# Performance work log

Measured on AMD Instinct MI355X. Metric: run time of the kernel, lower is better.

The kernel has to match this reference:

```python
import jax, jax.numpy as jnp
import numpy as np

HEADS = 16
DIM_HEAD = 64
QUERY_DIM = 1024
CONTEXT_DIM = 1024
INNER = HEADS * DIM_HEAD  # 1024


def setup_inputs() -> dict:
    key = jax.random.key(0)
    k1, k2, k3, k4, k5, k6, k7 = jax.random.split(key, 7)
    b, nq, nk = 2, 2048, 2048
    q = jax.random.normal(k1, (b, nq, QUERY_DIM), dtype=jnp.float32)
    context = jax.random.normal(k2, (b, nk, CONTEXT_DIM), dtype=jnp.float32)
    # True = masked out (filled with -inf); keep sparse so no row is fully masked
    mask = jax.random.randint(k3, (b, nk), 0, 2).astype(bool) & jax.random.randint(k7, (b, nk), 0, 2).astype(bool)
    s = 0.02
    Wq = jax.random.normal(k4, (QUERY_DIM, INNER), dtype=jnp.float32) * s
    Wkv = jax.random.normal(k5, (CONTEXT_DIM, 2 * INNER), dtype=jnp.float32) * s
    Wout = jax.random.normal(k6, (INNER, QUERY_DIM), dtype=jnp.float32) * s
    b_out = jnp.zeros((QUERY_DIM,), dtype=jnp.float32)
    return {"q": q, "context": context, "mask": mask, "Wq": Wq, "Wkv": Wkv, "Wout": Wout, "b_out": b_out}


def reference(q, context, mask, Wq, Wkv, Wout, b_out):
    b, nq, _ = q.shape
    nk = context.shape[1]
    h, dh = HEADS, DIM_HEAD
    scale = dh ** -0.5
    qp = q @ Wq                              # [b, nq, h*dh]
    k, v = jnp.split(context @ Wkv, 2, -1)   # each [b, nk, h*dh]
    qh = qp.reshape(b, nq, h, dh).transpose(0, 2, 1, 3)  # [b, h, nq, dh]
    kh = k.reshape(b, nk, h, dh).transpose(0, 2, 1, 3)
    vh = v.reshape(b, nk, h, dh).transpose(0, 2, 1, 3)
    attn = jnp.einsum('bhid,bhjd->bhij', qh, kh) * scale  # [b, h, nq, nk]
    attn = jnp.where(mask[:, None, None, :], -jnp.inf, attn)
    attn = jax.nn.softmax(attn, axis=-1)
    out = jnp.einsum('bhij,bhjd->bhid', attn, vh)         # [b, h, nq, dh]
    out = out.transpose(0, 2, 1, 3).reshape(b, nq, h * dh)
    return out @ Wout + b_out
```

## Files before the change

### kernel.cpp

```cpp
#include <hip/hip_runtime.h>
#include <hip/hip_bf16.h>
#include <stdint.h>
#include <math.h>

typedef unsigned short u16;
typedef __attribute__((ext_vector_type(8))) short bf16x8;
typedef __attribute__((ext_vector_type(4))) float f32x4;
typedef __attribute__((ext_vector_type(16))) float f32x16;
typedef __attribute__((ext_vector_type(4))) u16 u16x4;

#define DEVI __device__ __forceinline__

DEVI u16 f2bf(float x){
  uint32_t u = __float_as_uint(x);
  u += 0x7fffu + ((u >> 16) & 1u);
  return (u16)(u >> 16);
}

DEVI uint32_t pkbf2(float lo, float hi){
  union { __hip_bfloat162 h; uint32_t u; } x;
  x.h.x = __float2bfloat16(lo);
  x.h.y = __float2bfloat16(hi);
  return x.u;
}

DEVI void gload_lds16(const void* g, void* l){
  __builtin_amdgcn_global_load_lds((__attribute__((address_space(1))) const void*)g,
                                   (__attribute__((address_space(3))) void*)l,
                                   16, 0, 0);
}

DEVI void pl32swap_u(uint32_t& a, uint32_t& b){
  asm volatile("v_permlane32_swap_b32 %0, %1" : "+&v"(a), "+v"(b));
}

__global__ __launch_bounds__(256) void k_prep(const float* __restrict__ q,
                                              const float* __restrict__ ctx,
                                              const int* __restrict__ m,
                                              u16* __restrict__ qb, u16* __restrict__ cb,
                                              uint32_t* __restrict__ mb){
  const int b = blockIdx.x;
  if (b < 2048){
    const float* s = (b < 1024) ? q : ctx;
    u16* d = (b < 1024) ? qb : cb;
    const int base = (b & 1023) << 12;
    #pragma unroll
    for (int it = 0; it < 4; ++it){
      const int i = base + (it << 10) + (threadIdx.x << 2);
      const float4 v = *(const float4*)(s + i);
      u16x4 o = { f2bf(v.x), f2bf(v.y), f2bf(v.z), f2bf(v.w) };
      *(u16x4*)(d + i) = o;
    }
  } else {
    for (int w = threadIdx.x; w < 128; w += 256){
      const int bb = w >> 6, wi = w & 63;
      uint32_t bits = 0;
      for (int i = 0; i < 32; ++i) bits |= (m[(bb << 11) + (wi << 5) + i] ? 1u : 0u) << i;
      mb[w] = bits;
    }
  }
}

__global__ __launch_bounds__(256) void k_tr3(const float* __restrict__ Wq,
                                             const float* __restrict__ Wkv,
                                             const float* __restrict__ Wo,
                                             u16* __restrict__ WqT, u16* __restrict__ WkvT,
                                             u16* __restrict__ WoT){
  const int z = blockIdx.z;
  if (z != 1 && blockIdx.x >= 16) return;
  const float* s = (z == 0) ? Wq : (z == 1) ? Wkv : Wo;
  u16* d = (z == 0) ? WqT : (z == 1) ? WkvT : WoT;
  const int R = 1024, C = (z == 1) ? 2048 : 1024;
  __shared__ float t[64][65];
  const int x = threadIdx.x, y = threadIdx.y;
  const int r0 = blockIdx.y * 64, c0 = blockIdx.x * 64;
  #pragma unroll
  for (int yy = y; yy < 64; yy += 4) t[yy][x] = s[(size_t)(r0 + yy) * C + c0 + x];
  __syncthreads();
  #pragma unroll
  for (int yy = y; yy < 64; yy += 4) d[(size_t)(c0 + yy) * R + r0 + x] = f2bf(t[x][yy]);
}

__global__ __launch_bounds__(256, 2)
void k_gemm01(const u16* __restrict__ Aq, const u16* __restrict__ Ac,
              const u16* __restrict__ Bq, const u16* __restrict__ Bkv,
              u16* __restrict__ QPb, u16* __restrict__ Kbb, u16* __restrict__ Vtb)
{
  __shared__ __align__(16) u16 As[128 * 64];
  __shared__ __align__(16) u16 Bs[128 * 64];
  const int tid = threadIdx.x;
  const int lane = tid & 63, wave = tid >> 6;
  const int g = lane >> 4, l16 = lane & 15;
  const int bx = blockIdx.x;
  const bool isq = bx < 8;
  const u16* A = isq ? Aq : Ac;
  const u16* B = isq ? Bq : Bkv;
  const int brow = blockIdx.y << 7, bcol = (isq ? bx : bx - 8) << 7;
  const int wr = wave >> 1, wc = wave & 1;
  f32x4 acc[4][4] = {};

  for (int kt = 0; kt < 16; ++kt){
    const int k0 = kt << 6;
    #pragma unroll
    for (int i = 0; i < 4; ++i){
      const int c = i * 256 + tid;
      const int row = c >> 3;
      const int sc = ((c & 7) ^ (row & 7)) << 3;
      gload_lds16(A + (size_t)(brow + row) * 1024 + k0 + sc, (char*)As + (i * 4 + wave) * 1024);
      gload_lds16(B + (size_t)(bcol + row) * 1024 + k0 + sc, (char*)Bs + (i * 4 + wave) * 1024);
    }
    __syncthreads();
    #pragma unroll
    for (int kk = 0; kk < 2; ++kk){
      bf16x8 a[4], b[4];
      #pragma unroll
      for (int mi = 0; mi < 4; ++mi){
        const int r = wr * 64 + mi * 16 + l16;
        a[mi] = *(const bf16x8*)((const char*)As + r * 128 + (((kk << 6) + (g << 4)) ^ ((r & 7) << 4)));
      }
      #pragma unroll
      for (int ni = 0; ni < 4; ++ni){
        const int r = wc * 64 + ni * 16 + l16;
        b[ni] = *(const bf16x8*)((const char*)Bs + r * 128 + (((kk << 6) + (g << 4)) ^ ((r & 7) << 4)));
      }
      #pragma unroll
      for (int mi = 0; mi < 4; ++mi)
        #pragma unroll
        for (int ni = 0; ni < 4; ++ni)
          acc[mi][ni] = __builtin_amdgcn_mfma_f32_16x16x32_bf16(a[mi], b[ni], acc[mi][ni], 0, 0, 0);
    }
    __syncthreads();
  }

  #pragma unroll
  for (int mi = 0; mi < 4; ++mi){
    #pragma unroll
    for (int ni = 0; ni < 4; ++ni){
      #pragma unroll
      for (int r = 0; r < 4; ++r){
        const int row = brow + wr * 64 + mi * 16 + g * 4 + r;
        const int col = bcol + wc * 64 + ni * 16 + l16;
        const float v = acc[mi][ni][r];
        const int bb = row >> 11, qi = row & 2047;
        if (isq){
          const int h = col >> 6, dd = col & 63;
          QPb[(size_t)((bb << 4) + h) * 131072 + (qi << 6) + dd] = f2bf(v * 0.18033688f);
        } else if (col < 1024){
          const int h = col >> 6, dd = col & 63;
          Kbb[(size_t)((bb << 4) + h) * 131072 + (qi << 6) + dd] = f2bf(v);
        } else {
          const int c2 = col - 1024, h = c2 >> 6, dd = c2 & 63;
          Vtb[(size_t)((bb << 4) + h) * 131072 + (dd << 11) + qi] = f2bf(v);
        }
      }
    }
  }
}

__global__ __launch_bounds__(256, 2)
void k_gemm2(const u16* __restrict__ A, const u16* __restrict__ B,
             float* __restrict__ D, const float* __restrict__ bias)
{
  __shared__ __align__(16) u16 As[128 * 64];
  __shared__ __align__(16) u16 Bs[128 * 64];
  const int tid = threadIdx.x;
  const int lane = tid & 63, wave = tid >> 6;
  const int g = lane >> 4, l16 = lane & 15;
  const int brow = blockIdx.y << 7, bcol = blockIdx.x << 7;
  const int wr = wave >> 1, wc = wave & 1;
  f32x4 acc[4][4] = {};

  for (int kt = 0; kt < 16; ++kt){
    const int k0 = kt << 6;
    #pragma unroll
    for (int i = 0; i < 4; ++i){
      const int c = i * 256 + tid;
      const int row = c >> 3;
      const int sc = ((c & 7) ^ (row & 7)) << 3;
      gload_lds16(A + (size_t)(brow + row) * 1024 + k0 + sc, (char*)As + (i * 4 + wave) * 1024);
      gload_lds16(B + (size_t)(bcol + row) * 1024 + k0 + sc, (char*)Bs + (i * 4 + wave) * 1024);
    }
    __syncthreads();
    #pragma unroll
    for (int kk = 0; kk < 2; ++kk){
      bf16x8 a[4], b[4];
      #pragma unroll
      for (int mi = 0; mi < 4; ++mi){
        const int r = wr * 64 + mi * 16 + l16;
        a[mi] = *(const bf16x8*)((const char*)As + r * 128 + (((kk << 6) + (g << 4)) ^ ((r & 7) << 4)));
      }
      #pragma unroll
      for (int ni = 0; ni < 4; ++ni){
        const int r = wc * 64 + ni * 16 + l16;
        b[ni] = *(const bf16x8*)((const char*)Bs + r * 128 + (((kk << 6) + (g << 4)) ^ ((r & 7) << 4)));
      }
      #pragma unroll
      for (int mi = 0; mi < 4; ++mi)
        #pragma unroll
        for (int ni = 0; ni < 4; ++ni)
          acc[mi][ni] = __builtin_amdgcn_mfma_f32_16x16x32_bf16(a[mi], b[ni], acc[mi][ni], 0, 0, 0);
    }
    __syncthreads();
  }

  #pragma unroll
  for (int mi = 0; mi < 4; ++mi)
    #pragma unroll
    for (int ni = 0; ni < 4; ++ni)
      #pragma unroll
      for (int r = 0; r < 4; ++r){
        const int row = brow + wr * 64 + mi * 16 + g * 4 + r;
        const int col = bcol + wc * 64 + ni * 16 + l16;
        D[(size_t)row * 1024 + col] = acc[mi][ni][r] + bias[col];
      }
}

__global__ __launch_bounds__(128, 4)
void k_attn(const u16* __restrict__ QP, const u16* __restrict__ Kb,
            const u16* __restrict__ Vt, const uint32_t* __restrict__ mbits,
            u16* __restrict__ AO)
{
  __shared__ __align__(16) u16 Ks[2][64 * 64];
  __shared__ __align__(16) u16 Vs[2][64 * 64];
  const int tid = threadIdx.x, lane = tid & 63, wave = tid >> 6;
  const int l31 = lane & 31, hi = lane >> 5;
  const int bh = blockIdx.y;
  const int q0 = (blockIdx.x << 6) + (wave << 5);
  const u16* Qg = QP + (size_t)bh * 131072;
  const u16* Kg = Kb + (size_t)bh * 131072;
  const u16* Vg = Vt + (size_t)bh * 131072;
  const uint32_t* mrow = mbits + (bh >> 4) * 64;
  const int bpa = hi << 4;

  bf16x8 qf[4];
  #pragma unroll
  for (int ks = 0; ks < 4; ++ks)
    qf[ks] = *(const bf16x8*)(Qg + (size_t)(q0 + l31) * 64 + ks * 16 + hi * 8);

  f32x16 o0 = {}, o1 = {};
  float ls = 0.f;

  #pragma unroll
  for (int i = 0; i < 4; ++i){
    const int c = (i << 7) + tid;
    const int row = c >> 3;
    const int sc = ((c & 7) ^ (row & 7)) << 3;
    gload_lds16(Kg + (size_t)row * 64 + sc, (char*)Ks[0] + (i << 11) + (wave << 10));
    gload_lds16(Vg + (size_t)row * 2048 + sc, (char*)Vs[0] + (i << 11) + (wave << 10));
  }

  int cur = 0;
  for (int jt = 0; jt < 32; ++jt){
    const int j0 = jt << 6;
    __syncthreads();
    if (jt < 31){
      #pragma unroll
      for (int i = 0; i < 4; ++i){
        const int c = (i << 7) + tid;
        const int row = c >> 3;
        const int sc = ((c & 7) ^ (row & 7)) << 3;
        gload_lds16(Kg + (size_t)(j0 + 64 + row) * 64 + sc, (char*)Ks[cur ^ 1] + (i << 11) + (wave << 10));
        gload_lds16(Vg + (size_t)row * 2048 + j0 + 64 + sc, (char*)Vs[cur ^ 1] + (i << 11) + (wave << 10));
      }
    }

    f32x16 s0 = {}, s1 = {};
    __builtin_amdgcn_s_setprio(1);
    #pragma unroll
    for (int ks = 0; ks < 4; ++ks){
      const int co = ks * 32 + hi * 16;
      {
        const int r = l31;
        bf16x8 kf = *(const bf16x8*)((const char*)Ks[cur] + r * 128 + (co ^ ((r & 7) << 4)));
        s0 = __builtin_amdgcn_mfma_f32_32x32x16_bf16(kf, qf[ks], s0, 0, 0, 0);
      }
      {
        const int r = 32 + l31;
        bf16x8 kf = *(const bf16x8*)((const char*)Ks[cur] + r * 128 + (co ^ ((r & 7) << 4)));
        s1 = __builtin_amdgcn_mfma_f32_32x32x16_bf16(kf, qf[ks], s1, 0, 0, 0);
      }
    }
    __builtin_amdgcn_s_setprio(0);

    const uint32_t mw0 = mrow[(jt << 1) + 0] >> (hi << 2);
    const uint32_t mw1 = mrow[(jt << 1) + 1] >> (hi << 2);
    float rs = 0.f;
    #pragma unroll
    for (int r = 0; r < 16; ++r){
      const int c = (r & 3) + ((r >> 2) << 3);
      const float p0 = exp2f(fmaf((float)((mw0 >> c) & 1u), -3e38f, s0[r]));
      const float p1 = exp2f(fmaf((float)((mw1 >> c) & 1u), -3e38f, s1[r]));
      s0[r] = p0; s1[r] = p1;
      rs += p0 + p1;
    }
    rs += __shfl_xor(rs, 32);
    ls += rs;

    uint32_t w[4][4];
    #pragma unroll
    for (int t = 0; t < 2; ++t){
      { uint32_t A = pkbf2(s0[2*t], s0[2*t+1]),      B = pkbf2(s0[4+2*t],  s0[5+2*t]);
        pl32swap_u(A, B); w[0][t] = A; w[0][2+t] = B; }
      { uint32_t A = pkbf2(s0[8+2*t], s0[9+2*t]),    B = pkbf2(s0[12+2*t], s0[13+2*t]);
        pl32swap_u(A, B); w[1][t] = A; w[1][2+t] = B; }
      { uint32_t A = pkbf2(s1[2*t], s1[2*t+1]),      B = pkbf2(s1[4+2*t],  s1[5+2*t]);
        pl32swap_u(A, B); w[2][t] = A; w[2][2+t] = B; }
      { uint32_t A = pkbf2(s1[8+2*t], s1[9+2*t]),    B = pkbf2(s1[12+2*t], s1[13+2*t]);
        pl32swap_u(A, B); w[3][t] = A; w[3][2+t] = B; }
    }

    __builtin_amdgcn_s_setprio(1);
    #pragma unroll
    for (int ks = 0; ks < 4; ++ks){
      union { uint32_t u[4]; bf16x8 v; } pa;
      pa.u[0] = w[ks][0]; pa.u[1] = w[ks][1]; pa.u[2] = w[ks][2]; pa.u[3] = w[ks][3];
      const int co = ks * 32 + hi * 16;
      {
        const int r = l31;
        bf16x8 vf = *(const bf16x8*)((const char*)Vs[cur] + r * 128 + (co ^ ((r & 7) << 4)));
        o0 = __builtin_amdgcn_mfma_f32_32x32x16_bf16(pa.v, vf, o0, 0, 0, 0);
      }
      {
        const int r = 32 + l31;
        bf16x8 vf = *(const bf16x8*)((const char*)Vs[cur] + r * 128 + (co ^ ((r & 7) << 4)));
        o1 = __builtin_amdgcn_mfma_f32_32x32x16_bf16(pa.v, vf, o1, 0, 0, 0);
      }
    }
    __builtin_amdgcn_s_setprio(0);
    cur ^= 1;
  }

  const float linv = 1.0f / ls;
  const int b = bh >> 4, h = bh & 15;
  #pragma unroll
  for (int r = 0; r < 16; ++r){
    const int c = (r & 3) + ((r >> 2) << 3);
    const float lr = __int_as_float(__builtin_amdgcn_ds_bpermute(bpa + (c << 2), __float_as_int(linv)));
    const int qi = q0 + c + (hi << 2);
    AO[(size_t)(b * 2048 + qi) * 1024 + h * 64 + l31]      = f2bf(o0[r] * lr);
    AO[(size_t)(b * 2048 + qi) * 1024 + h * 64 + 32 + l31] = f2bf(o1[r] * lr);
  }
}

extern "C" void kernel_launch(void* const* d_in, const int* in_sizes, int n_in,
                              void* d_out, int out_size, void* d_ws, size_t ws_size,
                              hipStream_t stream)
{
  (void)in_sizes; (void)n_in; (void)out_size; (void)ws_size;
  const float* q   = (const float*)d_in[0];
  const float* ctx = (const float*)d_in[1];
  const int*   msk = (const int*)d_in[2];
  const float* Wq  = (const float*)d_in[3];
  const float* Wkv = (const float*)d_in[4];
  const float* Wo  = (const float*)d_in[5];
  const float* bo  = (const float*)d_in[6];
  float* out = (float*)d_out;

  char* ws = (char*)d_ws;
  u16*      q_bf  = (u16*)(ws);
  u16*      c_bf  = (u16*)(ws + (size_t)( 8u << 20));
  u16*      WqT   = (u16*)(ws + (size_t)(16u << 20));
  u16*      WkvT  = (u16*)(ws + (size_t)(18u << 20));
  u16*      WoT   = (u16*)(ws + (size_t)(22u << 20));
  uint32_t* mbits = (uint32_t*)(ws + (size_t)(24u << 20));
  u16*      QPb   = (u16*)(ws + (size_t)(25u << 20));
  u16*      Kbb   = (u16*)(ws + (size_t)(33u << 20));
  u16*      Vtb   = (u16*)(ws + (size_t)(41u << 20));
  u16*      AOb   = (u16*)(ws + (size_t)(49u << 20));

  k_prep  <<<dim3(2049),      dim3(256),   0, stream>>>(q, ctx, msk, q_bf, c_bf, mbits);
  k_tr3   <<<dim3(32, 16, 3), dim3(64, 4), 0, stream>>>(Wq, Wkv, Wo, WqT, WkvT, WoT);
  k_gemm01<<<dim3(24, 32),    dim3(256),   0, stream>>>(q_bf, c_bf, WqT, WkvT, QPb, Kbb, Vtb);
  k_attn  <<<dim3(32, 32),    dim3(128),   0, stream>>>(QPb, Kbb, Vtb, mbits, AOb);
  k_gemm2 <<<dim3(8, 32),     dim3(256),   0, stream>>>(AOb, WoT, out, bo);
}
```

Baseline: 259.5 us.

## Widen attention blocks to four waves, shrink output GEMM tile, cheapen softmax masking

```diff
diff --git a/kernel.cpp b/kernel.cpp
--- a/kernel.cpp
+++ b/kernel.cpp
@@ -1,5 +1,4 @@
 #include <hip/hip_runtime.h>
-#include <hip/hip_bf16.h>
 #include <stdint.h>
 #include <math.h>
 
@@ -17,11 +16,10 @@
   return (u16)(u >> 16);
 }
 
-DEVI uint32_t pkbf2(float lo, float hi){
-  union { __hip_bfloat162 h; uint32_t u; } x;
-  x.h.x = __float2bfloat16(lo);
-  x.h.y = __float2bfloat16(hi);
-  return x.u;
+DEVI uint32_t cvtpk(float lo, float hi){
+  uint32_t w;
+  asm("v_cvt_pk_bf16_f32 %0, %1, %2" : "=v"(w) : "v"(lo), "v"(hi));
+  return w;
 }
 
 DEVI void gload_lds16(const void* g, void* l){
@@ -162,13 +160,12 @@
              float* __restrict__ D, const float* __restrict__ bias)
 {
   __shared__ __align__(16) u16 As[128 * 64];
-  __shared__ __align__(16) u16 Bs[128 * 64];
+  __shared__ __align__(16) u16 Bs[64 * 64];
   const int tid = threadIdx.x;
   const int lane = tid & 63, wave = tid >> 6;
   const int g = lane >> 4, l16 = lane & 15;
-  const int brow = blockIdx.y << 7, bcol = blockIdx.x << 7;
-  const int wr = wave >> 1, wc = wave & 1;
-  f32x4 acc[4][4] = {};
+  const int brow = blockIdx.y << 7, bcol = blockIdx.x << 6;
+  f32x4 acc[2][4] = {};
 
   for (int kt = 0; kt < 16; ++kt){
     const int k0 = kt << 6;
@@ -178,24 +175,30 @@
       const int row = c >> 3;
       const int sc = ((c & 7) ^ (row & 7)) << 3;
       gload_lds16(A + (size_t)(brow + row) * 1024 + k0 + sc, (char*)As + (i * 4 + wave) * 1024);
+    }
+    #pragma unroll
+    for (int i = 0; i < 2; ++i){
+      const int c = i * 256 + tid;
+      const int row = c >> 3;
+      const int sc = ((c & 7) ^ (row & 7)) << 3;
       gload_lds16(B + (size_t)(bcol + row) * 1024 + k0 + sc, (char*)Bs + (i * 4 + wave) * 1024);
     }
     __syncthreads();
     #pragma unroll
     for (int kk = 0; kk < 2; ++kk){
-      bf16x8 a[4], b[4];
-      #pragma unroll
-      for (int mi = 0; mi < 4; ++mi){
-        const int r = wr * 64 + mi * 16 + l16;
+      bf16x8 a[2], b[4];
+      #pragma unroll
+      for (int mi = 0; mi < 2; ++mi){
+        const int r = wave * 32 + mi * 16 + l16;
         a[mi] = *(const bf16x8*)((const char*)As + r * 128 + (((kk << 6) + (g << 4)) ^ ((r & 7) << 4)));
       }
       #pragma unroll
       for (int ni = 0; ni < 4; ++ni){
-        const int r = wc * 64 + ni * 16 + l16;
+        const int r = ni * 16 + l16;
         b[ni] = *(const bf16x8*)((const char*)Bs + r * 128 + (((kk << 6) + (g << 4)) ^ ((r & 7) << 4)));
       }
       #pragma unroll
-      for (int mi = 0; mi < 4; ++mi)
+      for (int mi = 0; mi < 2; ++mi)
         #pragma unroll
         for (int ni = 0; ni < 4; ++ni)
           acc[mi][ni] = __builtin_amdgcn_mfma_f32_16x16x32_bf16(a[mi], b[ni], acc[mi][ni], 0, 0, 0);
@@ -204,18 +207,18 @@
   }
 
   #pragma unroll
-  for (int mi = 0; mi < 4; ++mi)
+  for (int mi = 0; mi < 2; ++mi)
     #pragma unroll
     for (int ni = 0; ni < 4; ++ni)
       #pragma unroll
       for (int r = 0; r < 4; ++r){
-        const int row = brow + wr * 64 + mi * 16 + g * 4 + r;
-        const int col = bcol + wc * 64 + ni * 16 + l16;
+        const int row = brow + wave * 32 + mi * 16 + g * 4 + r;
+        const int col = bcol + ni * 16 + l16;
         D[(size_t)row * 1024 + col] = acc[mi][ni][r] + bias[col];
       }
 }
 
-__global__ __launch_bounds__(128, 4)
+__global__ __launch_bounds__(256, 2)
 void k_attn(const u16* __restrict__ QP, const u16* __restrict__ Kb,
             const u16* __restrict__ Vt, const uint32_t* __restrict__ mbits,
             u16* __restrict__ AO)
@@ -225,7 +228,7 @@
   const int tid = threadIdx.x, lane = tid & 63, wave = tid >> 6;
   const int l31 = lane & 31, hi = lane >> 5;
   const int bh = blockIdx.y;
-  const int q0 = (blockIdx.x << 6) + (wave << 5);
+  const int q0 = (blockIdx.x << 7) + (wave << 5);
   const u16* Qg = QP + (size_t)bh * 131072;
   const u16* Kg = Kb + (size_t)bh * 131072;
   const u16* Vg = Vt + (size_t)bh * 131072;
@@ -241,12 +244,12 @@
   float ls = 0.f;
 
   #pragma unroll
-  for (int i = 0; i < 4; ++i){
-    const int c = (i << 7) + tid;
+  for (int i = 0; i < 2; ++i){
+    const int c = (i << 8) + tid;
     const int row = c >> 3;
     const int sc = ((c & 7) ^ (row & 7)) << 3;
-    gload_lds16(Kg + (size_t)row * 64 + sc, (char*)Ks[0] + (i << 11) + (wave << 10));
-    gload_lds16(Vg + (size_t)row * 2048 + sc, (char*)Vs[0] + (i << 11) + (wave << 10));
+    gload_lds16(Kg + (size_t)row * 64 + sc, (char*)Ks[0] + (i * 4 + wave) * 1024);
+    gload_lds16(Vg + (size_t)row * 2048 + sc, (char*)Vs[0] + (i * 4 + wave) * 1024);
   }
 
   int cur = 0;
@@ -255,12 +258,12 @@
     __syncthreads();
     if (jt < 31){
       #pragma unroll
-      for (int i = 0; i < 4; ++i){
-        const int c = (i << 7) + tid;
+      for (int i = 0; i < 2; ++i){
+        const int c = (i << 8) + tid;
         const int row = c >> 3;
         const int sc = ((c & 7) ^ (row & 7)) << 3;
-        gload_lds16(Kg + (size_t)(j0 + 64 + row) * 64 + sc, (char*)Ks[cur ^ 1] + (i << 11) + (wave << 10));
-        gload_lds16(Vg + (size_t)row * 2048 + j0 + 64 + sc, (char*)Vs[cur ^ 1] + (i << 11) + (wave << 10));
+        gload_lds16(Kg + (size_t)(j0 + 64 + row) * 64 + sc, (char*)Ks[cur ^ 1] + (i * 4 + wave) * 1024);
+        gload_lds16(Vg + (size_t)row * 2048 + j0 + 64 + sc, (char*)Vs[cur ^ 1] + (i * 4 + wave) * 1024);
       }
     }
 
@@ -282,14 +285,16 @@
     }
     __builtin_amdgcn_s_setprio(0);
 
-    const uint32_t mw0 = mrow[(jt << 1) + 0] >> (hi << 2);
-    const uint32_t mw1 = mrow[(jt << 1) + 1] >> (hi << 2);
+    const uint32_t nmw0 = ~(mrow[(jt << 1) + 0] >> (hi << 2));
+    const uint32_t nmw1 = ~(mrow[(jt << 1) + 1] >> (hi << 2));
     float rs = 0.f;
     #pragma unroll
     for (int r = 0; r < 16; ++r){
       const int c = (r & 3) + ((r >> 2) << 3);
-      const float p0 = exp2f(fmaf((float)((mw0 >> c) & 1u), -3e38f, s0[r]));
-      const float p1 = exp2f(fmaf((float)((mw1 >> c) & 1u), -3e38f, s1[r]));
+      const uint32_t am0 = (uint32_t)(((int)(nmw0 << (31 - c))) >> 31);
+      const uint32_t am1 = (uint32_t)(((int)(nmw1 << (31 - c))) >> 31);
+      const float p0 = __uint_as_float(__float_as_uint(exp2f(s0[r])) & am0);
+      const float p1 = __uint_as_float(__float_as_uint(exp2f(s1[r])) & am1);
       s0[r] = p0; s1[r] = p1;
       rs += p0 + p1;
     }
@@ -299,13 +304,13 @@
     uint32_t w[4][4];
     #pragma unroll
     for (int t = 0; t < 2; ++t){
-      { uint32_t A = pkbf2(s0[2*t], s0[2*t+1]),      B = pkbf2(s0[4+2*t],  s0[5+2*t]);
+      { uint32_t A = cvtpk(s0[2*t], s0[2*t+1]),      B = cvtpk(s0[4+2*t],  s0[5+2*t]);
         pl32swap_u(A, B); w[0][t] = A; w[0][2+t] = B; }
-      { uint32_t A = pkbf2(s0[8+2*t], s0[9+2*t]),    B = pkbf2(s0[12+2*t], s0[13+2*t]);
+      { uint32_t A = cvtpk(s0[8+2*t], s0[9+2*t]),    B = cvtpk(s0[12+2*t], s0[13+2*t]);
         pl32swap_u(A, B); w[1][t] = A; w[1][2+t] = B; }
-      { uint32_t A = pkbf2(s1[2*t], s1[2*t+1]),      B = pkbf2(s1[4+2*t],  s1[5+2*t]);
+      { uint32_t A = cvtpk(s1[2*t], s1[2*t+1]),      B = cvtpk(s1[4+2*t],  s1[5+2*t]);
         pl32swap_u(A, B); w[2][t] = A; w[2][2+t] = B; }
-      { uint32_t A = pkbf2(s1[8+2*t], s1[9+2*t]),    B = pkbf2(s1[12+2*t], s1[13+2*t]);
+      { uint32_t A = cvtpk(s1[8+2*t], s1[9+2*t]),    B = cvtpk(s1[12+2*t], s1[13+2*t]);
         pl32swap_u(A, B); w[3][t] = A; w[3][2+t] = B; }
     }
 
@@ -371,6 +376,6 @@
   k_prep  <<<dim3(2049),      dim3(256),   0, stream>>>(q, ctx, msk, q_bf, c_bf, mbits);
   k_tr3   <<<dim3(32, 16, 3), dim3(64, 4), 0, stream>>>(Wq, Wkv, Wo, WqT, WkvT, WoT);
   k_gemm01<<<dim3(24, 32),    dim3(256),   0, stream>>>(q_bf, c_bf, WqT, WkvT, QPb, Kbb, Vtb);
-  k_attn  <<<dim3(32, 32),    dim3(128),   0, stream>>>(QPb, Kbb, Vtb, mbits, AOb);
-  k_gemm2 <<<dim3(8, 32),     dim3(256),   0, stream>>>(AOb, WoT, out, bo);
-}
+  k_attn  <<<dim3(16, 32),    dim3(256),   0, stream>>>(QPb, Kbb, Vtb, mbits, AOb);
+  k_gemm2 <<<dim3(16, 32),    dim3(256),   0, stream>>>(AOb, WoT, out, bo);
+}
```

Result: faster. 222.6 us (-14.2%).
